# Performance work log

Hardware: AMD Instinct MI355X
Metric: run time of the kernel (lower is better)

Reference implementation:

```python
import jax, jax.numpy as jnp
from jax import lax
import numpy as np

LEVELS = 3
HU_RANGE = 240.0 - (-160.0)          # hu_window = (-160, 240)
BASE_THR = 40.0 / HU_RANGE           # threshold / hu_range
MAD_TO_SIGMA = 1.0 / 0.6745


def haar2(x):
    """Single-level 2D orthonormal Haar DWT. x: [B, h, w] (h, w even).
    Returns cA, cH, cV, cD each [B, h//2, w//2]. Sign conventions are
    irrelevant to this loss (only |coeff| matters in MAD and L1 terms)."""
    B, h, w = x.shape
    x = x.reshape(B, h // 2, 2, w // 2, 2)
    a = x[:, :, 0, :, 0]
    b = x[:, :, 0, :, 1]
    c = x[:, :, 1, :, 0]
    d = x[:, :, 1, :, 1]
    cA = (a + b + c + d) * 0.5
    cH = (a + b - c - d) * 0.5
    cV = (a - b + c - d) * 0.5
    cD = (a - b - c + d) * 0.5
    return cA, cH, cV, cD


def soft_threshold(c, t):
    return jnp.sign(c) * jnp.maximum(jnp.abs(c) - t, 0.0)


def setup_inputs() -> dict:
    key = jax.random.key(0)
    pred = jax.random.normal(key, (128, 1, 512, 512), dtype=jnp.float32)
    return {"pred": pred}


def reference(pred):
    x = pred[:, 0]                     # [B, H, W]
    B = x.shape[0]

    # Multi-level decomposition: details[0] = finest, details[-1] = coarsest.
    details = []
    cA = x
    for _ in range(LEVELS):
        cA, cH, cV, cD = haar2(cA)
        details.append((cH, cV, cD))

    # pywt coeffs[1] is the COARSEST detail triple -> MAD noise estimate.
    cH, cV, cD = details[-1]
    all_details = jnp.concatenate(
        [cH.reshape(B, -1), cV.reshape(B, -1), cD.reshape(B, -1)], axis=1)
    sigma = jnp.median(jnp.abs(all_details), axis=1) * MAD_TO_SIGMA  # [B]
    adaptive_thr = jnp.clip(sigma * 2.5, BASE_THR * 0.5, BASE_THR * 2.0)
    adaptive_thr = lax.stop_gradient(adaptive_thr)                   # [B]

    # level_idx = 1 corresponds to pywt coeffs[1] (coarsest) = details[-1].
    total = jnp.zeros((B,), dtype=x.dtype)
    for level_idx in range(1, LEVELS + 1):
        cH, cV, cD = details[LEVELS - level_idx]
        t = (adaptive_thr / (2.0 ** (level_idx - 1)))[:, None, None]
        lvl = jnp.zeros((B,), dtype=x.dtype)
        for c in (cH, cV, cD):
            target = lax.stop_gradient(soft_threshold(c, t))
            lvl = lvl + jnp.mean(jnp.abs(c - target), axis=(1, 2))
        total = total + (1.0 / level_idx) * lvl / 3.0

    loss = jnp.mean(total)             # sum over batch / valid_samples (all valid)
    avg_noise = jnp.mean(sigma)
    return loss, avg_noise
```

## Files before the change

kernel.cpp:

```cpp
#include <hip/hip_runtime.h>
#include <stdint.h>


static constexpr int BATCH = 128;
static constexpr int W = 512;
static constexpr int NBIN = 512;

__device__ __forceinline__ float block_reduce_sum(float v, float* lds) {
    #pragma unroll
    for (int off = 32; off > 0; off >>= 1)
        v += __shfl_down(v, off, 64);
    const int lane = threadIdx.x & 63;
    const int wave = threadIdx.x >> 6;
    if (lane == 0) lds[wave] = v;
    __syncthreads();
    if (threadIdx.x == 0) {
        float s = 0.0f;
        for (int w = 0; w < 4; ++w) s += lds[w];
        lds[0] = s;
    }
    __syncthreads();
    const float r = lds[0];
    __syncthreads();
    return r;
}

__device__ __forceinline__ void haar_quad(float a, float b, float c, float d,
                                          float& cA, float& cH, float& cV, float& cD) {
    const float sab = a + b, scd = c + d, dab = a - b, dcd = c - d;
    cA = 0.5f * (sab + scd);
    cH = 0.5f * (sab - scd);
    cV = 0.5f * (dab + dcd);
    cD = 0.5f * (dab - dcd);
}

__device__ __forceinline__ float wavelet_block_loss(
        const float* __restrict__ blk, float t1, float t2, float t3) {
    float cA1[4][4];
    float s1 = 0.0f, s2 = 0.0f, s3 = 0.0f;
    #pragma unroll
    for (int rr = 0; rr < 4; ++rr) {
        const float4 r0a = *(const float4*)(blk + (size_t)(2 * rr) * W);
        const float4 r0b = *(const float4*)(blk + (size_t)(2 * rr) * W + 4);
        const float4 r1a = *(const float4*)(blk + (size_t)(2 * rr + 1) * W);
        const float4 r1b = *(const float4*)(blk + (size_t)(2 * rr + 1) * W + 4);
        const float top[8] = {r0a.x, r0a.y, r0a.z, r0a.w, r0b.x, r0b.y, r0b.z, r0b.w};
        const float bot[8] = {r1a.x, r1a.y, r1a.z, r1a.w, r1b.x, r1b.y, r1b.z, r1b.w};
        #pragma unroll
        for (int cc = 0; cc < 4; ++cc) {
            float cA, cH, cV, cD;
            haar_quad(top[2*cc], top[2*cc+1], bot[2*cc], bot[2*cc+1], cA, cH, cV, cD);
            s1 += fminf(fabsf(cH), t1) + fminf(fabsf(cV), t1) + fminf(fabsf(cD), t1);
            cA1[rr][cc] = cA;
        }
    }
    float cA2[2][2];
    #pragma unroll
    for (int rr = 0; rr < 2; ++rr)
        #pragma unroll
        for (int cc = 0; cc < 2; ++cc) {
            float cA, cH, cV, cD;
            haar_quad(cA1[2*rr][2*cc], cA1[2*rr][2*cc+1],
                      cA1[2*rr+1][2*cc], cA1[2*rr+1][2*cc+1], cA, cH, cV, cD);
            s2 += fminf(fabsf(cH), t2) + fminf(fabsf(cV), t2) + fminf(fabsf(cD), t2);
            cA2[rr][cc] = cA;
        }
    {
        float cA, cH, cV, cD;
        haar_quad(cA2[0][0], cA2[0][1], cA2[1][0], cA2[1][1], cA, cH, cV, cD);
        s3 = fminf(fabsf(cH), t3) + fminf(fabsf(cV), t3) + fminf(fabsf(cD), t3);
    }
    const float w1 = 1.0f / (9.0f * 65536.0f);
    const float w2 = 1.0f / (6.0f * 16384.0f);
    const float w3 = 1.0f / (3.0f * 4096.0f);
    return s1 * w1 + s2 * w2 + s3 * w3;
}

__global__ __launch_bounds__(256) void pass_a(const float* __restrict__ x,
                                              float* __restrict__ partials,
                                              uint32_t* __restrict__ ghist,
                                              float* __restrict__ out) {
    __shared__ uint32_t h[NBIN];
    __shared__ float lds[8];
    const int tid  = threadIdx.x;
    const int lane = tid & 63;
    const int wv   = tid >> 6;
    const int sub  = blockIdx.x;
    const int b    = blockIdx.y;

    h[tid] = 0u;
    h[tid + 256] = 0u;
    if (sub == 0 && b == 0 && tid < 2) out[tid] = 0.0f;
    __syncthreads();

    const float BASE = 40.0f / 400.0f;
    const float t3 = BASE * 2.0f, t2 = t3 * 0.5f, t1 = t3 * 0.25f;

    const int R = sub * 4 + wv;
    const float* strip = x + (size_t)b * W * W + (size_t)(R * 8) * W;

    float cA1A[4][2], cA1B[4][2];
    float s1 = 0.0f, s2 = 0.0f, s3 = 0.0f;

    #pragma unroll
    for (int rp = 0; rp < 4; ++rp) {
        const float* r0 = strip + (size_t)(2 * rp) * W;
        const float* r1 = strip + (size_t)(2 * rp + 1) * W;
        const float4 tA = *(const float4*)(r0 + 4 * lane);
        const float4 bA = *(const float4*)(r1 + 4 * lane);
        const float4 tB = *(const float4*)(r0 + 256 + 4 * lane);
        const float4 bB = *(const float4*)(r1 + 256 + 4 * lane);

        float cA, cH, cV, cD;
        haar_quad(tA.x, tA.y, bA.x, bA.y, cA, cH, cV, cD);
        s1 += fminf(fabsf(cH), t1) + fminf(fabsf(cV), t1) + fminf(fabsf(cD), t1);
        cA1A[rp][0] = cA;
        haar_quad(tA.z, tA.w, bA.z, bA.w, cA, cH, cV, cD);
        s1 += fminf(fabsf(cH), t1) + fminf(fabsf(cV), t1) + fminf(fabsf(cD), t1);
        cA1A[rp][1] = cA;
        haar_quad(tB.x, tB.y, bB.x, bB.y, cA, cH, cV, cD);
        s1 += fminf(fabsf(cH), t1) + fminf(fabsf(cV), t1) + fminf(fabsf(cD), t1);
        cA1B[rp][0] = cA;
        haar_quad(tB.z, tB.w, bB.z, bB.w, cA, cH, cV, cD);
        s1 += fminf(fabsf(cH), t1) + fminf(fabsf(cV), t1) + fminf(fabsf(cD), t1);
        cA1B[rp][1] = cA;
    }

    float cA2A[2], cA2B[2];
    #pragma unroll
    for (int j = 0; j < 2; ++j) {
        float cA, cH, cV, cD;
        haar_quad(cA1A[2*j][0], cA1A[2*j][1], cA1A[2*j+1][0], cA1A[2*j+1][1],
                  cA, cH, cV, cD);
        s2 += fminf(fabsf(cH), t2) + fminf(fabsf(cV), t2) + fminf(fabsf(cD), t2);
        cA2A[j] = cA;
        haar_quad(cA1B[2*j][0], cA1B[2*j][1], cA1B[2*j+1][0], cA1B[2*j+1][1],
                  cA, cH, cV, cD);
        s2 += fminf(fabsf(cH), t2) + fminf(fabsf(cV), t2) + fminf(fabsf(cD), t2);
        cA2B[j] = cA;
    }

    const float pA0 = __shfl_xor(cA2A[0], 1, 64);
    const float pA1 = __shfl_xor(cA2A[1], 1, 64);
    const float pB0 = __shfl_xor(cA2B[0], 1, 64);
    const float pB1 = __shfl_xor(cA2B[1], 1, 64);
    if ((lane & 1) == 0) {
        float cA, cH, cV, cD;
        haar_quad(cA2A[0], pA0, cA2A[1], pA1, cA, cH, cV, cD);
        float aH = fabsf(cH), aV = fabsf(cV), aD = fabsf(cD);
        s3 += fminf(aH, t3) + fminf(aV, t3) + fminf(aD, t3);
        atomicAdd(&h[min((int)(aH * 256.0f), NBIN - 1)], 1u);
        atomicAdd(&h[min((int)(aV * 256.0f), NBIN - 1)], 1u);
        atomicAdd(&h[min((int)(aD * 256.0f), NBIN - 1)], 1u);
        haar_quad(cA2B[0], pB0, cA2B[1], pB1, cA, cH, cV, cD);
        aH = fabsf(cH); aV = fabsf(cV); aD = fabsf(cD);
        s3 += fminf(aH, t3) + fminf(aV, t3) + fminf(aD, t3);
        atomicAdd(&h[min((int)(aH * 256.0f), NBIN - 1)], 1u);
        atomicAdd(&h[min((int)(aV * 256.0f), NBIN - 1)], 1u);
        atomicAdd(&h[min((int)(aD * 256.0f), NBIN - 1)], 1u);
    }

    const float w1 = 1.0f / (9.0f * 65536.0f);
    const float w2 = 1.0f / (6.0f * 16384.0f);
    const float w3 = 1.0f / (3.0f * 4096.0f);
    const float part = s1 * w1 + s2 * w2 + s3 * w3;

    const float tot = block_reduce_sum(part, lds);
    if (tid == 0) partials[b * 16 + sub] = tot;

    uint32_t* gh = ghist + ((size_t)b * 16 + sub) * NBIN;
    gh[tid] = h[tid];
    gh[tid + 256] = h[tid + 256];
}

__global__ __launch_bounds__(64) void pass_b(const uint32_t* __restrict__ ghist,
                                             const float* __restrict__ partials,
                                             const float* __restrict__ x,
                                             float* __restrict__ out) {
    const int b = blockIdx.x;
    const int lane = threadIdx.x;
    uint32_t c[8] = {0, 0, 0, 0, 0, 0, 0, 0};

    #pragma unroll 4
    for (int s = 0; s < 16; ++s) {
        const uint32_t* hb = ghist + ((size_t)b * 16 + s) * NBIN + lane * 8;
        const uint4 u0 = *(const uint4*)(hb);
        const uint4 u1 = *(const uint4*)(hb + 4);
        c[0] += u0.x; c[1] += u0.y; c[2] += u0.z; c[3] += u0.w;
        c[4] += u1.x; c[5] += u1.y; c[6] += u1.z; c[7] += u1.w;
    }

    uint32_t lane_sum = 0;
    #pragma unroll
    for (int j = 0; j < 8; ++j) lane_sum += c[j];

    uint32_t incl = lane_sum;
    #pragma unroll
    for (int off = 1; off < 64; off <<= 1) {
        const uint32_t v = __shfl_up(incl, off, 64);
        if (lane >= off) incl += v;
    }
    uint32_t run = incl - lane_sum;

    int bin1 = 0x7FFFFFFF, bin2 = 0x7FFFFFFF;
    #pragma unroll
    for (int j = 0; j < 8; ++j) {
        const uint32_t nxt = run + c[j];
        if (run < 6144u && nxt >= 6144u) bin1 = lane * 8 + j;
        if (run < 6145u && nxt >= 6145u) bin2 = lane * 8 + j;
        run = nxt;
    }
    #pragma unroll
    for (int off = 32; off > 0; off >>= 1) {
        bin1 = min(bin1, __shfl_down(bin1, off, 64));
        bin2 = min(bin2, __shfl_down(bin2, off, 64));
    }
    bin1 = __shfl(bin1, 0, 64);
    bin2 = __shfl(bin2, 0, 64);

    const float v1 = ((float)bin1 + 0.5f) * (1.0f / 256.0f);
    const float v2 = ((float)bin2 + 0.5f) * (1.0f / 256.0f);
    const float med = 0.5f * (v1 + v2);
    const float sig = med * (float)(1.0 / 0.6745);
    const float BASE = 40.0f / 400.0f;
    const float TTOP = BASE * 2.0f;
    const float t = fminf(fmaxf(sig * 2.5f, BASE * 0.5f), TTOP);

    float loss_b;
    if (t == TTOP) {
        float v = (lane < 16) ? partials[b * 16 + lane] : 0.0f;
        #pragma unroll
        for (int off = 32; off > 0; off >>= 1) v += __shfl_down(v, off, 64);
        loss_b = v;
    } else {
        float part = 0.0f;
        #pragma unroll 1
        for (int k = 0; k < 64; ++k) {
            const int p = k * 64 + lane;
            const int i3 = p >> 6, j3 = p & 63;
            const float* blk = x + (size_t)b * W * W + (size_t)(i3 * 8) * W + j3 * 8;
            part += wavelet_block_loss(blk, t * 0.25f, t * 0.5f, t);
        }
        #pragma unroll
        for (int off = 32; off > 0; off >>= 1) part += __shfl_down(part, off, 64);
        loss_b = part;
    }

    if (lane == 0) {
        atomicAdd(&out[0], loss_b * (1.0f / (float)BATCH));
        atomicAdd(&out[1], sig * (1.0f / (float)BATCH));
    }
}

extern "C" void kernel_launch(void* const* d_in, const int* in_sizes, int n_in,
                              void* d_out, int out_size, void* d_ws, size_t ws_size,
                              hipStream_t stream) {
    const float* x = (const float*)d_in[0];
    float* ws = (float*)d_ws;
    float* partials = ws;
    uint32_t* ghist = (uint32_t*)(ws + 2048);

    dim3 grid(16, BATCH);
    pass_a<<<grid, 256, 0, stream>>>(x, partials, ghist, (float*)d_out);
    pass_b<<<BATCH, 64, 0, stream>>>(ghist, partials, x, (float*)d_out);
}
```

Baseline: 192.0 us.

## Fuse histogram and median passes into one cooperative kernel with grid sync

```diff
diff --git a/kernel.cpp b/kernel.cpp
--- a/kernel.cpp
+++ b/kernel.cpp
@@ -1,5 +1,8 @@
 #include <hip/hip_runtime.h>
+#include <hip/hip_cooperative_groups.h>
 #include <stdint.h>
+
+namespace cg = cooperative_groups;
 
 
 static constexpr int BATCH = 128;
@@ -76,32 +79,13 @@
     return s1 * w1 + s2 * w2 + s3 * w3;
 }
 
-__global__ __launch_bounds__(256) void pass_a(const float* __restrict__ x,
-                                              float* __restrict__ partials,
-                                              uint32_t* __restrict__ ghist,
-                                              float* __restrict__ out) {
-    __shared__ uint32_t h[NBIN];
-    __shared__ float lds[8];
-    const int tid  = threadIdx.x;
-    const int lane = tid & 63;
-    const int wv   = tid >> 6;
-    const int sub  = blockIdx.x;
-    const int b    = blockIdx.y;
-
-    h[tid] = 0u;
-    h[tid + 256] = 0u;
-    if (sub == 0 && b == 0 && tid < 2) out[tid] = 0.0f;
-    __syncthreads();
-
-    const float BASE = 40.0f / 400.0f;
-    const float t3 = BASE * 2.0f, t2 = t3 * 0.5f, t1 = t3 * 0.25f;
-
-    const int R = sub * 4 + wv;
-    const float* strip = x + (size_t)b * W * W + (size_t)(R * 8) * W;
-
+__device__ __forceinline__ void strip_work(const float* __restrict__ base,
+                                           int R, int lane,
+                                           float t1, float t2, float t3,
+                                           float& s1, float& s2, float& s3,
+                                           uint32_t* h) {
+    const float* strip = base + (size_t)(R * 8) * W;
     float cA1A[4][2], cA1B[4][2];
-    float s1 = 0.0f, s2 = 0.0f, s3 = 0.0f;
-
     #pragma unroll
     for (int rp = 0; rp < 4; ++rp) {
         const float* r0 = strip + (size_t)(2 * rp) * W;
@@ -110,7 +94,6 @@
         const float4 bA = *(const float4*)(r1 + 4 * lane);
         const float4 tB = *(const float4*)(r0 + 256 + 4 * lane);
         const float4 bB = *(const float4*)(r1 + 256 + 4 * lane);
-
         float cA, cH, cV, cD;
         haar_quad(tA.x, tA.y, bA.x, bA.y, cA, cH, cV, cD);
         s1 += fminf(fabsf(cH), t1) + fminf(fabsf(cV), t1) + fminf(fabsf(cD), t1);
@@ -125,7 +108,6 @@
         s1 += fminf(fabsf(cH), t1) + fminf(fabsf(cV), t1) + fminf(fabsf(cD), t1);
         cA1B[rp][1] = cA;
     }
-
     float cA2A[2], cA2B[2];
     #pragma unroll
     for (int j = 0; j < 2; ++j) {
@@ -139,7 +121,6 @@
         s2 += fminf(fabsf(cH), t2) + fminf(fabsf(cV), t2) + fminf(fabsf(cD), t2);
         cA2B[j] = cA;
     }
-
     const float pA0 = __shfl_xor(cA2A[0], 1, 64);
     const float pA1 = __shfl_xor(cA2A[1], 1, 64);
     const float pB0 = __shfl_xor(cA2B[0], 1, 64);
@@ -159,6 +140,34 @@
         atomicAdd(&h[min((int)(aV * 256.0f), NBIN - 1)], 1u);
         atomicAdd(&h[min((int)(aD * 256.0f), NBIN - 1)], 1u);
     }
+}
+
+__global__ __launch_bounds__(256, 2) void wavelet_coop(
+        const float* __restrict__ x, float* __restrict__ partials,
+        uint32_t* __restrict__ ghist, float* __restrict__ out) {
+    __shared__ uint32_t h[NBIN];
+    __shared__ float lds[8];
+    const int tid  = threadIdx.x;
+    const int lane = tid & 63;
+    const int wv   = tid >> 6;
+    const int xb   = blockIdx.x;
+    const int b    = blockIdx.y;
+
+    h[tid] = 0u;
+    h[tid + 256] = 0u;
+    if (xb == 0 && b == 0 && tid < 2) out[tid] = 0.0f;
+    __syncthreads();
+
+    const float BASE = 40.0f / 400.0f;
+    const float t3 = BASE * 2.0f, t2 = t3 * 0.5f, t1 = t3 * 0.25f;
+    const float* base = x + (size_t)b * W * W;
+
+    float s1 = 0.0f, s2 = 0.0f, s3 = 0.0f;
+    #pragma unroll 1
+    for (int k = 0; k < 4; ++k) {
+        const int sub = xb * 4 + k;
+        strip_work(base, sub * 4 + wv, lane, t1, t2, t3, s1, s2, s3, h);
+    }
 
     const float w1 = 1.0f / (9.0f * 65536.0f);
     const float w2 = 1.0f / (6.0f * 16384.0f);
@@ -166,8 +175,103 @@
     const float part = s1 * w1 + s2 * w2 + s3 * w3;
 
     const float tot = block_reduce_sum(part, lds);
+    if (tid == 0) partials[b * 4 + xb] = tot;
+
+    uint32_t* gh = ghist + ((size_t)b * 4 + xb) * NBIN;
+    gh[tid] = h[tid];
+    gh[tid + 256] = h[tid + 256];
+
+    cg::this_grid().sync();
+
+    if (xb != 0 || tid >= 64) return;
+
+    uint32_t c[8] = {0, 0, 0, 0, 0, 0, 0, 0};
+    #pragma unroll
+    for (int s = 0; s < 4; ++s) {
+        const uint32_t* hb = ghist + ((size_t)b * 4 + s) * NBIN + lane * 8;
+        const uint4 u0 = *(const uint4*)(hb);
+        const uint4 u1 = *(const uint4*)(hb + 4);
+        c[0] += u0.x; c[1] += u0.y; c[2] += u0.z; c[3] += u0.w;
+        c[4] += u1.x; c[5] += u1.y; c[6] += u1.z; c[7] += u1.w;
+    }
+    uint32_t lane_sum = 0;
+    #pragma unroll
+    for (int j = 0; j < 8; ++j) lane_sum += c[j];
+    uint32_t incl = lane_sum;
+    #pragma unroll
+    for (int off = 1; off < 64; off <<= 1) {
+        const uint32_t v = __shfl_up(incl, off, 64);
+        if (lane >= off) incl += v;
+    }
+    uint32_t run = incl - lane_sum;
+    int bin1 = 0x7FFFFFFF, bin2 = 0x7FFFFFFF;
+    #pragma unroll
+    for (int j = 0; j < 8; ++j) {
+        const uint32_t nxt = run + c[j];
+        if (run < 6144u && nxt >= 6144u) bin1 = lane * 8 + j;
+        if (run < 6145u && nxt >= 6145u) bin2 = lane * 8 + j;
+        run = nxt;
+    }
+    #pragma unroll
+    for (int off = 32; off > 0; off >>= 1) {
+        bin1 = min(bin1, __shfl_down(bin1, off, 64));
+        bin2 = min(bin2, __shfl_down(bin2, off, 64));
+    }
+    bin1 = __shfl(bin1, 0, 64);
+    bin2 = __shfl(bin2, 0, 64);
+
+    const float v1 = ((float)bin1 + 0.5f) * (1.0f / 256.0f);
+    const float v2 = ((float)bin2 + 0.5f) * (1.0f / 256.0f);
+    const float med = 0.5f * (v1 + v2);
+    const float sig = med * (float)(1.0 / 0.6745);
+    const float TTOP = BASE * 2.0f;
+    const float t = fminf(fmaxf(sig * 2.5f, BASE * 0.5f), TTOP);
+
+    float loss_b;
+    if (t == TTOP) {
+        float v = (lane < 4) ? partials[b * 4 + lane] : 0.0f;
+        #pragma unroll
+        for (int off = 32; off > 0; off >>= 1) v += __shfl_down(v, off, 64);
+        loss_b = v;
+    } else {
+        float part2 = 0.0f;
+        #pragma unroll 1
+        for (int k = 0; k < 64; ++k) {
+            const int p = k * 64 + lane;
+            const int i3 = p >> 6, j3 = p & 63;
+            const float* blk = base + (size_t)(i3 * 8) * W + j3 * 8;
+            part2 += wavelet_block_loss(blk, t * 0.25f, t * 0.5f, t);
+        }
+        #pragma unroll
+        for (int off = 32; off > 0; off >>= 1) part2 += __shfl_down(part2, off, 64);
+        loss_b = part2;
+    }
+    if (lane == 0) {
+        atomicAdd(&out[0], loss_b * (1.0f / (float)BATCH));
+        atomicAdd(&out[1], sig * (1.0f / (float)BATCH));
+    }
+}
+
+__global__ __launch_bounds__(256) void pass_a(const float* __restrict__ x,
+                                              float* __restrict__ partials,
+                                              uint32_t* __restrict__ ghist,
+                                              float* __restrict__ out) {
+    __shared__ uint32_t h[NBIN];
+    __shared__ float lds[8];
+    const int tid = threadIdx.x, lane = tid & 63, wv = tid >> 6;
+    const int sub = blockIdx.x, b = blockIdx.y;
+    h[tid] = 0u; h[tid + 256] = 0u;
+    if (sub == 0 && b == 0 && tid < 2) out[tid] = 0.0f;
+    __syncthreads();
+    const float BASE = 40.0f / 400.0f;
+    const float t3 = BASE * 2.0f, t2 = t3 * 0.5f, t1 = t3 * 0.25f;
+    float s1 = 0.0f, s2 = 0.0f, s3 = 0.0f;
+    strip_work(x + (size_t)b * W * W, sub * 4 + wv, lane, t1, t2, t3, s1, s2, s3, h);
+    const float w1 = 1.0f / (9.0f * 65536.0f);
+    const float w2 = 1.0f / (6.0f * 16384.0f);
+    const float w3 = 1.0f / (3.0f * 4096.0f);
+    const float tot = block_reduce_sum(s1 * w1 + s2 * w2 + s3 * w3, lds);
     if (tid == 0) partials[b * 16 + sub] = tot;
-
     uint32_t* gh = ghist + ((size_t)b * 16 + sub) * NBIN;
     gh[tid] = h[tid];
     gh[tid + 256] = h[tid + 256];
@@ -180,7 +284,6 @@
     const int b = blockIdx.x;
     const int lane = threadIdx.x;
     uint32_t c[8] = {0, 0, 0, 0, 0, 0, 0, 0};
-
     #pragma unroll 4
     for (int s = 0; s < 16; ++s) {
         const uint32_t* hb = ghist + ((size_t)b * 16 + s) * NBIN + lane * 8;
@@ -189,11 +292,9 @@
         c[0] += u0.x; c[1] += u0.y; c[2] += u0.z; c[3] += u0.w;
         c[4] += u1.x; c[5] += u1.y; c[6] += u1.z; c[7] += u1.w;
     }
-
     uint32_t lane_sum = 0;
     #pragma unroll
     for (int j = 0; j < 8; ++j) lane_sum += c[j];
-
     uint32_t incl = lane_sum;
     #pragma unroll
     for (int off = 1; off < 64; off <<= 1) {
@@ -201,7 +302,6 @@
         if (lane >= off) incl += v;
     }
     uint32_t run = incl - lane_sum;
-
     int bin1 = 0x7FFFFFFF, bin2 = 0x7FFFFFFF;
     #pragma unroll
     for (int j = 0; j < 8; ++j) {
@@ -217,7 +317,6 @@
     }
     bin1 = __shfl(bin1, 0, 64);
     bin2 = __shfl(bin2, 0, 64);
-
     const float v1 = ((float)bin1 + 0.5f) * (1.0f / 256.0f);
     const float v2 = ((float)bin2 + 0.5f) * (1.0f / 256.0f);
     const float med = 0.5f * (v1 + v2);
@@ -225,7 +324,6 @@
     const float BASE = 40.0f / 400.0f;
     const float TTOP = BASE * 2.0f;
     const float t = fminf(fmaxf(sig * 2.5f, BASE * 0.5f), TTOP);
-
     float loss_b;
     if (t == TTOP) {
         float v = (lane < 16) ? partials[b * 16 + lane] : 0.0f;
@@ -245,7 +343,6 @@
         for (int off = 32; off > 0; off >>= 1) part += __shfl_down(part, off, 64);
         loss_b = part;
     }
-
     if (lane == 0) {
         atomicAdd(&out[0], loss_b * (1.0f / (float)BATCH));
         atomicAdd(&out[1], sig * (1.0f / (float)BATCH));
@@ -256,11 +353,20 @@
                               void* d_out, int out_size, void* d_ws, size_t ws_size,
                               hipStream_t stream) {
     const float* x = (const float*)d_in[0];
+    float* out = (float*)d_out;
     float* ws = (float*)d_ws;
-    float* partials = ws;
-    uint32_t* ghist = (uint32_t*)(ws + 2048);
-
-    dim3 grid(16, BATCH);
-    pass_a<<<grid, 256, 0, stream>>>(x, partials, ghist, (float*)d_out);
-    pass_b<<<BATCH, 64, 0, stream>>>(ghist, partials, x, (float*)d_out);
-}
+
+    float*    partials4 = ws;
+    uint32_t* ghist4    = (uint32_t*)(ws + 512);
+    float*    partials16= ws + 262656;
+    uint32_t* ghist16   = (uint32_t*)(ws + 264704);
+
+    void* args[] = {(void*)&x, (void*)&partials4, (void*)&ghist4, (void*)&out};
+    const hipError_t e = hipLaunchCooperativeKernel(
+        (const void*)wavelet_coop, dim3(4, BATCH), dim3(256), args, 0, stream);
+    if (e != hipSuccess) {
+        dim3 grid(16, BATCH);
+        pass_a<<<grid, 256, 0, stream>>>(x, partials16, ghist16, out);
+        pass_b<<<BATCH, 64, 0, stream>>>(ghist16, partials16, x, out);
+    }
+}
```

Measured after the change: 252.3 us. 31.4% more time.
